# Optimization experiments

Measured on AMD Instinct MI355X. Metric: run time of the kernel, lower is better.

Reference implementation:

```python
import jax, jax.numpy as jnp
import numpy as np

NUM_LEVELS = 4
RADIUS = 4


def _avg_pool2(x):
    # x: [N, H, W] -> [N, H//2, W//2], 2x2 mean pool, stride 2 (F.avg_pool2d(corr,2,2))
    N, H, W = x.shape
    return x.reshape(N, H // 2, 2, W // 2, 2).mean(axis=(2, 4))


def _bilinear_sample(img, x, y):
    # img: [N, H, W]; x, y: [N, P] pixel coords.
    # Matches F.grid_sample(..., mode='bilinear', align_corners=True, padding_mode='zeros')
    # after the pixel->normalized->pixel round trip in bilinear_sampler (identity).
    N, H, W = img.shape
    x0 = jnp.floor(x)
    y0 = jnp.floor(y)
    wx = x - x0
    wy = y - y0
    x0i = x0.astype(jnp.int32)
    y0i = y0.astype(jnp.int32)
    flat = img.reshape(N, H * W)

    def gather(yi, xi):
        valid = (xi >= 0) & (xi <= W - 1) & (yi >= 0) & (yi <= H - 1)
        idx = jnp.clip(yi, 0, H - 1) * W + jnp.clip(xi, 0, W - 1)
        v = jnp.take_along_axis(flat, idx, axis=1)
        return jnp.where(valid, v, jnp.zeros((), img.dtype))

    v00 = gather(y0i, x0i)
    v01 = gather(y0i, x0i + 1)
    v10 = gather(y0i + 1, x0i)
    v11 = gather(y0i + 1, x0i + 1)
    return (v00 * (1 - wy) * (1 - wx) + v01 * (1 - wy) * wx
            + v10 * wy * (1 - wx) + v11 * wy * wx)


def _corr_block(fmap1, fmap2, coords):
    B, D, H, W = fmap1.shape
    # all-pairs correlation: [B, H*W, H*W] / sqrt(D)
    f1 = fmap1.reshape(B, D, H * W)
    f2 = fmap2.reshape(B, D, H * W)
    corr = jnp.einsum('bdn,bdm->bnm', f1, f2) / jnp.sqrt(jnp.asarray(D, fmap1.dtype))
    corr = corr.reshape(B * H * W, H, W)
    pyramid = [corr]
    for _ in range(NUM_LEVELS - 1):
        corr = _avg_pool2(corr)
        pyramid.append(corr)

    # coords: [B, 2, H, W] (x, y) -> [B*H*W, 2]
    c = coords.transpose(0, 2, 3, 1).reshape(B * H * W, 2)
    r = RADIUS
    d = jnp.linspace(-r, r, 2 * r + 1)
    dyg, dxg = jnp.meshgrid(d, d, indexing='ij')
    # faithful to torch: delta = stack(meshgrid(dy, dx), -1); channel 0 added to x, 1 to y
    delta = jnp.stack([dyg, dxg], axis=-1).reshape(-1, 2)  # [81, 2]

    outs = []
    for i, lvl in enumerate(pyramid):
        cl = c[:, None, :] / (2.0 ** i) + delta[None, :, :]  # [N, 81, 2]
        s = _bilinear_sample(lvl, cl[..., 0], cl[..., 1])    # [N, 81]
        outs.append(s.reshape(B, H, W, (2 * r + 1) ** 2))
    out = jnp.concatenate(outs, axis=-1)                     # [B, H, W, 4*81]
    return out.transpose(0, 3, 1, 2).astype(jnp.float32)


def setup_inputs() -> dict:
    key = jax.random.key(0)
    k1, k2, k3 = jax.random.split(key, 3)
    B, D, H, W = 2, 256, 80, 80
    fmap1 = jax.random.normal(k1, (B, D, H, W), dtype=jnp.float32)
    fmap2 = jax.random.normal(k2, (B, D, H, W), dtype=jnp.float32)
    # pixel coords in [0, W-1] x [0, H-1] (channel 0 = x, channel 1 = y)
    u = jax.random.uniform(k3, (B, 2, H, W), dtype=jnp.float32)
    scale = jnp.asarray([W - 1, H - 1], jnp.float32).reshape(1, 2, 1, 1)
    coords = u * scale
    return {"fmap1": fmap1, "fmap2": fmap2, "coords": coords}


def reference(fmap1, fmap2, coords):
    return _corr_block(fmap1, fmap2, coords)
```

## Files before the change

### kernel.cpp

```cpp
#include <hip/hip_runtime.h>


typedef _Float16 h2 __attribute__((ext_vector_type(2)));
typedef _Float16 half8 __attribute__((ext_vector_type(8)));
typedef float f32x4 __attribute__((ext_vector_type(4)));

#define HWDIM 80
#define DCH 256
#define NPIX 12800
#define NBUCKET 800
#define CHP 352

__global__ __launch_bounds__(256) void zero_k(float4* __restrict__ dst) {
    int i = blockIdx.x * 256 + threadIdx.x;
    dst[i] = make_float4(0.f, 0.f, 0.f, 0.f);
}

__global__ __launch_bounds__(256) void transpose_all(const float* __restrict__ f1,
                                                     const float* __restrict__ f2,
                                                     _Float16* __restrict__ f1h,
                                                     _Float16* __restrict__ f2p0) {
    __shared__ float tile[256][33];
    int bid = blockIdx.x;
    bool isf1 = bid < 400;
    int lb = isf1 ? bid : bid - 400;
    const float* src = isf1 ? f1 : f2;
    int b = lb / 200;
    int s0 = (lb % 200) * 32;
    int t = threadIdx.x;
    const float* sb = src + (size_t)b * DCH * (HWDIM * HWDIM);
#pragma unroll 4
    for (int k = 0; k < 32; ++k) {
        int j = t + 256 * k;
        int c = j >> 5, s = j & 31;
        tile[c][s] = sb[(size_t)c * (HWDIM * HWDIM) + s0 + s];
    }
    __syncthreads();
    int p = t & 127;
    int srow = t >> 7;
    if (isf1) {
        _Float16* db = f1h + ((size_t)b * 6400 + s0) * DCH;
#pragma unroll 4
        for (int k = 0; k < 16; ++k) {
            int s = 2 * k + srow;
            h2 v;
            v[0] = (_Float16)tile[2 * p][s];
            v[1] = (_Float16)tile[2 * p + 1][s];
            *(h2*)(db + (size_t)s * DCH + 2 * p) = v;
        }
    } else {
#pragma unroll 4
        for (int k = 0; k < 16; ++k) {
            int s = 2 * k + srow;
            int spatial = s0 + s;
            int yy = spatial / 80;
            int xx = spatial - yy * 80;
            h2 v;
            v[0] = (_Float16)tile[2 * p][s];
            v[1] = (_Float16)tile[2 * p + 1][s];
            size_t off = (size_t)b * 2073600 + (size_t)(p >> 4) * 259200
                       + ((size_t)(yy + 5) * 90 + (xx + 5)) * 32 + ((2 * p) & 31);
            *(h2*)(f2p0 + off) = v;
        }
    }
}

__global__ __launch_bounds__(256) void pools(const _Float16* __restrict__ l0,
                                             _Float16* __restrict__ l1,
                                             _Float16* __restrict__ l2,
                                             _Float16* __restrict__ l3) {
    int i = blockIdx.x * 256 + threadIdx.x;
    if (i < 409600) {
        int c2 = i & 15;
        int r = i >> 4;
        int x = r % 40; r /= 40;
        int y = r % 40; r /= 40;
        int pl = r & 7;
        int b = r >> 3;
        const h2* s = (const h2*)l0 + (size_t)b * 1036800 + (size_t)pl * 129600
                    + ((size_t)(2 * y + 5) * 90 + (2 * x + 5)) * 16 + c2;
        h2 v00 = s[0], v01 = s[16], v10 = s[90 * 16], v11 = s[90 * 16 + 16];
        float r0 = ((float)v00[0] + (float)v01[0] + (float)v10[0] + (float)v11[0]) * 0.25f;
        float r1 = ((float)v00[1] + (float)v01[1] + (float)v10[1] + (float)v11[1]) * 0.25f;
        h2 o; o[0] = (_Float16)r0; o[1] = (_Float16)r1;
        *((h2*)l1 + (size_t)b * 320000 + (size_t)pl * 40000
          + ((size_t)(y + 5) * 50 + (x + 5)) * 16 + c2) = o;
    } else if (i < 512000) {
        int j = i - 409600;
        int c2 = j & 15;
        int r = j >> 4;
        int x = r % 20; r /= 20;
        int y = r % 20; r /= 20;
        int pl = r & 7;
        int b = r >> 3;
        const h2* s = (const h2*)l0 + (size_t)b * 1036800 + (size_t)pl * 129600 + c2;
        float r0 = 0.f, r1 = 0.f;
#pragma unroll
        for (int dy = 0; dy < 4; ++dy)
#pragma unroll
            for (int dx = 0; dx < 4; ++dx) {
                h2 v = s[((size_t)(4 * y + dy + 5) * 90 + (4 * x + dx + 5)) * 16];
                r0 += (float)v[0];
                r1 += (float)v[1];
            }
        h2 o; o[0] = (_Float16)(r0 * 0.0625f); o[1] = (_Float16)(r1 * 0.0625f);
        *((h2*)l2 + (size_t)b * 115200 + (size_t)pl * 14400
          + ((size_t)(y + 5) * 30 + (x + 5)) * 16 + c2) = o;
    } else {
        int j = i - 512000;
        int c2 = j & 15;
        int r = j >> 4;
        int x = r % 10; r /= 10;
        int y = r % 10; r /= 10;
        int pl = r & 7;
        int b = r >> 3;
        const h2* s = (const h2*)l0 + (size_t)b * 1036800 + (size_t)pl * 129600 + c2;
        float r0 = 0.f, r1 = 0.f;
#pragma unroll
        for (int dy = 0; dy < 8; ++dy)
#pragma unroll
            for (int dx = 0; dx < 8; ++dx) {
                h2 v = s[((size_t)(8 * y + dy + 5) * 90 + (8 * x + dx + 5)) * 16];
                r0 += (float)v[0];
                r1 += (float)v[1];
            }
        h2 o; o[0] = (_Float16)(r0 * 0.015625f); o[1] = (_Float16)(r1 * 0.015625f);
        *((h2*)l3 + (size_t)b * 51200 + (size_t)pl * 6400
          + ((size_t)(y + 5) * 20 + (x + 5)) * 16 + c2) = o;
    }
}

static __device__ __forceinline__ int bucket_of(const float* coords, int n) {
    int b = n / 6400;
    int r = n - b * 6400;
    float cx = coords[(size_t)b * 12800 + r];
    float cy = coords[(size_t)b * 12800 + 6400 + r];
    int ix = min(max((int)floorf(cx), 0), 79);
    int iy = min(max((int)floorf(cy), 0), 79);
    return b * 400 + (iy >> 2) * 20 + (ix >> 2);
}

__global__ __launch_bounds__(1024) void bucket_k(const float* __restrict__ coords,
                                                 int* __restrict__ sortedIdxP,
                                                 int* __restrict__ rank) {
    __shared__ unsigned int histS[NBUCKET], startS[NBUCKET], curS[NBUCKET];
    __shared__ unsigned int waveSum[16];
    __shared__ unsigned int totalS;
    int t = threadIdx.x;
    if (t < NBUCKET) histS[t] = 0u;
    __syncthreads();
    int bkt[13];
#pragma unroll
    for (int i = 0; i < 13; ++i) {
        int n = i * 1024 + t;
        if (n < NPIX) {
            bkt[i] = bucket_of(coords, n);
            atomicAdd(&histS[bkt[i]], 1u);
        }
    }
    __syncthreads();
    unsigned int v = (t < NBUCKET) ? ((histS[t] + 15u) & ~15u) : 0u;
    unsigned int x = v;
#pragma unroll
    for (int d = 1; d < 64; d <<= 1) {
        unsigned int y = __shfl_up(x, d);
        if ((t & 63) >= d) x += y;
    }
    if ((t & 63) == 63) waveSum[t >> 6] = x;
    __syncthreads();
    if (t < 16) {
        unsigned int w = waveSum[t];
#pragma unroll
        for (int d = 1; d < 16; d <<= 1) {
            unsigned int y = __shfl_up(w, d);
            if (t >= d) w += y;
        }
        waveSum[t] = w;
    }
    __syncthreads();
    unsigned int incl = x + ((t >> 6) ? waveSum[(t >> 6) - 1] : 0u);
    if (t < NBUCKET) {
        unsigned int e = incl - v;
        startS[t] = e;
        curS[t] = e;
        if (t == NBUCKET - 1) totalS = incl;
    }
    __syncthreads();
#pragma unroll
    for (int i = 0; i < 13; ++i) {
        int n = i * 1024 + t;
        if (n < NPIX) {
            unsigned int pos = atomicAdd(&curS[bkt[i]], 1u);
            sortedIdxP[pos] = n;
            rank[n] = (int)pos;
        }
    }
    __syncthreads();
    if (t < NBUCKET) {
        unsigned int h = histS[t];
        if (h) {
            unsigned int pc = (h + 15u) & ~15u;
            unsigned int base = startS[t];
            int dup = sortedIdxP[base];
            for (unsigned int s = h; s < pc; ++s) sortedIdxP[base + s] = dup;
        }
    }
    for (unsigned int s = totalS + t; s < 25600u; s += 1024u) sortedIdxP[s] = -1;
}

template <int TB, int TE>
static __device__ __forceinline__ void run_tiles(
    int lane, int b,
    const _Float16* __restrict__ f2p0, const _Float16* __restrict__ f2p1,
    const _Float16* __restrict__ f2p2, const _Float16* __restrict__ f2p3,
    const int* X0cS, const int* Y0cS, const half8* bf, _Float16* G) {
#pragma unroll
    for (int tt = TB; tt < TE; ++tt) {
        const int L  = tt < 11 ? 0 : tt < 19 ? 1 : tt < 26 ? 2 : 3;
        const int rt = tt - (L == 0 ? 0 : L == 1 ? 11 : L == 2 ? 19 : 26);
        const int Ww = L == 0 ? 13 : L == 1 ? 11 : 10;
        const int MT = L == 0 ? 169 : L == 1 ? 121 : 100;
        const int MAG = L == 0 ? 161320 : L == 1 ? 190652 : 209716;
        const int Wp = L == 0 ? 90 : L == 1 ? 50 : L == 2 ? 30 : 20;
        const int PS = L == 0 ? 259200 : L == 1 ? 80000 : L == 2 ? 28800 : 12800;
        const int PB = L == 0 ? 2073600 : L == 1 ? 640000 : L == 2 ? 230400 : 102400;
        const int GO = L == 0 ? 0 : L == 1 ? 176 : L == 2 ? 304 : 416;
        const _Float16* f2L = (L == 0 ? f2p0 : L == 1 ? f2p1 : L == 2 ? f2p2 : f2p3);
        const _Float16* f2b = f2L + (size_t)b * PB
                            + ((size_t)(Y0cS[L] + 5) * Wp + (X0cS[L] + 5)) * 32;
        int m = min(rt * 16 + (lane & 15), MT - 1);
        int my = (m * MAG) >> 21;
        int mx = m - my * Ww;
        const float4* ap = (const float4*)(f2b + (size_t)(my * Wp + mx) * 32)
                         + (lane >> 4);
        half8 av[8];
#pragma unroll
        for (int kk = 0; kk < 8; ++kk)
            av[kk] = __builtin_bit_cast(half8, ap[kk * (PS / 8)]);
        __builtin_amdgcn_sched_barrier(0);
        f32x4 acc0 = {0.f, 0.f, 0.f, 0.f};
        f32x4 acc1 = {0.f, 0.f, 0.f, 0.f};
#pragma unroll
        for (int kk = 0; kk < 8; kk += 2) {
            acc0 = __builtin_amdgcn_mfma_f32_16x16x32_f16(av[kk], bf[kk], acc0, 0, 0, 0);
            acc1 = __builtin_amdgcn_mfma_f32_16x16x32_f16(av[kk + 1], bf[kk + 1], acc1, 0, 0, 0);
        }
        int gr = GO + rt * 16 + (lane >> 4) * 4;
#pragma unroll
        for (int r = 0; r < 4; ++r)
            G[(gr + r) * 17 + (lane & 15)] = (_Float16)(acc0[r] + acc1[r]);
    }
}

__global__ __launch_bounds__(512, 4) void corr_mfma(
    const _Float16* __restrict__ f1h,
    const _Float16* __restrict__ f2p0, const _Float16* __restrict__ f2p1,
    const _Float16* __restrict__ f2p2, const _Float16* __restrict__ f2p3,
    const float* __restrict__ coords, const int* __restrict__ sortedIdxP,
    _Float16* __restrict__ scratch) {
    __shared__ _Float16 G[528 * 17];
    __shared__ _Float16 f1S[16 * 264];
    __shared__ float fxS[4][16], fyS[4][16];
    __shared__ int lxS[4][16], lyS[4][16];
    __shared__ int X0cS[4], Y0cS[4], bS;

    int pphys = blockIdx.x;
    int l = (pphys & 7) * 200 + (pphys >> 3);
    int tid = threadIdx.x;
    if (sortedIdxP[l * 16] < 0) return;
    int lane = tid & 63;
    int wave = tid >> 6;

    {
        int px = tid >> 5, q = tid & 31;
        int n = sortedIdxP[l * 16 + px];
        const float4* src = (const float4*)(f1h + (size_t)n * DCH);
        *((float4*)(f1S + px * 264) + q) = src[q];
    }
    if (tid < 64) {
        int px = tid & 15, Lt = tid >> 4;
        int n = sortedIdxP[l * 16 + px];
        int b = n / 6400;
        int r = n - b * 6400;
        float cx = coords[(size_t)b * 12800 + r];
        float cy = coords[(size_t)b * 12800 + 6400 + r];
        float ls = 1.0f / (float)(1 << Lt);
        float cxl = cx * ls, cyl = cy * ls;
        float fxf = floorf(cxl), fyf = floorf(cyl);
        int X0 = (int)fxf - 4, Y0 = (int)fyf - 4;
        int ix = min(max((int)floorf(cx), 0), 79);
        int iy = min(max((int)floorf(cy), 0), 79);
        int X0c = (((ix >> 2) * 4) >> Lt) - 4;
        int Y0c = (((iy >> 2) * 4) >> Lt) - 4;
        lxS[Lt][px] = min(max(X0 - X0c, 0), 3);
        lyS[Lt][px] = min(max(Y0 - Y0c, 0), 3);
        fxS[Lt][px] = cxl - fxf;
        fyS[Lt][px] = cyl - fyf;
        X0cS[Lt] = X0c;
        Y0cS[Lt] = Y0c;
        if (tid == 0) bS = sortedIdxP[l * 16] / 6400;
    }
    __syncthreads();
    int b = bS;

    half8 bf[8];
#pragma unroll
    for (int kk = 0; kk < 8; ++kk)
        bf[kk] = *(const half8*)(f1S + (lane & 15) * 264 + ((lane >> 4) + 4 * kk) * 8);

    if      (wave == 0) run_tiles<0, 5>(lane, b, f2p0, f2p1, f2p2, f2p3, X0cS, Y0cS, bf, G);
    else if (wave == 1) run_tiles<5, 9>(lane, b, f2p0, f2p1, f2p2, f2p3, X0cS, Y0cS, bf, G);
    else if (wave == 2) run_tiles<9, 13>(lane, b, f2p0, f2p1, f2p2, f2p3, X0cS, Y0cS, bf, G);
    else if (wave == 3) run_tiles<13, 17>(lane, b, f2p0, f2p1, f2p2, f2p3, X0cS, Y0cS, bf, G);
    else if (wave == 4) run_tiles<17, 21>(lane, b, f2p0, f2p1, f2p2, f2p3, X0cS, Y0cS, bf, G);
    else if (wave == 5) run_tiles<21, 25>(lane, b, f2p0, f2p1, f2p2, f2p3, X0cS, Y0cS, bf, G);
    else if (wave == 6) run_tiles<25, 29>(lane, b, f2p0, f2p1, f2p2, f2p3, X0cS, Y0cS, bf, G);
    else                run_tiles<29, 33>(lane, b, f2p0, f2p1, f2p2, f2p3, X0cS, Y0cS, bf, G);
    __syncthreads();

    _Float16* sc = scratch + (size_t)l * 16 * CHP;
    for (int idx = tid; idx < 5184; idx += 512) {
        int k2 = idx >> 4, x = idx & 15;
        int Le = (k2 * 810) >> 16;
        int k = k2 - Le * 81;
        int Ww = Le == 0 ? 13 : Le == 1 ? 11 : 10;
        int GO = Le == 0 ? 0 : Le == 1 ? 176 : Le == 2 ? 304 : 416;
        int a = (k * 57) >> 9;
        int c = k - 9 * a;
        int gx = lxS[Le][x] + a, gy = lyS[Le][x] + c;
        int m00 = GO + gy * Ww + gx;
        float fx = fxS[Le][x], fy = fyS[Le][x];
        float t00 = (float)G[m00 * 17 + x];
        float t01 = (float)G[(m00 + 1) * 17 + x];
        float t10 = (float)G[(m00 + Ww) * 17 + x];
        float t11 = (float)G[(m00 + Ww + 1) * 17 + x];
        float v = ((1.f - fy) * ((1.f - fx) * t00 + fx * t01)
                 + fy * ((1.f - fx) * t10 + fx * t11)) * 0.0625f;
        sc[x * CHP + k2] = (_Float16)v;
    }
}

__global__ __launch_bounds__(256) void unsort_t(const _Float16* __restrict__ scratch,
                                                const int* __restrict__ rank,
                                                float* __restrict__ out) {
    __shared__ _Float16 lds[64][40];
    int blk = blockIdx.x;
    int b = blk / 100;
    int nl0 = (blk % 100) * 64;
    int t = threadIdx.x;
    int p = t >> 2, j = t & 3;
    int n = blk * 64 + p;
    int rk = rank[n];
    const float4* src = (const float4*)(scratch + (size_t)rk * CHP);
    int px = t & 63, iq = t >> 6;

    for (int c = 0; c < 11; ++c) {
        float4 f4 = src[c * 4 + j];
        *(float4*)(&lds[p][j * 8]) = f4;
        __syncthreads();
#pragma unroll
        for (int w = 0; w < 8; ++w) {
            int i = w * 4 + iq;
            int ch = c * 32 + i;
            if (ch < 324)
                out[((size_t)b * 324 + ch) * 6400 + nl0 + px] = (float)lds[px][i];
        }
        __syncthreads();
    }
}

extern "C" void kernel_launch(void* const* d_in, const int* in_sizes, int n_in,
                              void* d_out, int out_size, void* d_ws, size_t ws_size,
                              hipStream_t stream) {
    const float* fmap1 = (const float*)d_in[0];
    const float* fmap2 = (const float*)d_in[1];
    const float* coords = (const float*)d_in[2];
    float* out = (float*)d_out;
    char* ws = (char*)d_ws;

    _Float16* f1h  = (_Float16*)(ws);
    _Float16* f2p0 = (_Float16*)(ws + 6553600);
    _Float16* f2p1 = (_Float16*)(ws + 14848000);
    _Float16* f2p2 = (_Float16*)(ws + 17408000);
    _Float16* f2p3 = (_Float16*)(ws + 18329600);
    int* sortedIdxP = (int*)(ws + 18739200);
    int* rank       = (int*)(ws + 18841600);
    _Float16* scratch = (_Float16*)(ws + 18892800);

    zero_k<<<dim3(2975), dim3(256), 0, stream>>>((float4*)f2p0);

    transpose_all<<<dim3(800), dim3(256), 0, stream>>>(fmap1, fmap2, f1h, f2p0);
    pools<<<dim3(2100), dim3(256), 0, stream>>>(f2p0, f2p1, f2p2, f2p3);
    bucket_k<<<dim3(1), dim3(1024), 0, stream>>>(coords, sortedIdxP, rank);
    corr_mfma<<<dim3(1600), dim3(512), 0, stream>>>(f1h, f2p0, f2p1, f2p2, f2p3,
                                                    coords, sortedIdxP, scratch);
    unsort_t<<<dim3(200), dim3(256), 0, stream>>>(scratch, rank, out);
}
```

Measured before the change: 98.22 us.

## Stage f2 planes through LDS with double-buffered async loads per pyramid level

Replaces per-wave direct global loads of all eight K-planes with cooperative global_load_lds staging into a swizzled double-buffered LDS plane, processing pyramid levels one at a time. The G buffer shrinks to a single level and launch bounds ask for more blocks per CU, trading register-held operands for LDS traffic and many more block-wide barriers. The sampling epilogue is split per level. The aim is better overlap of global loads with MFMA and higher occupancy, at the cost of extra synchronization and idle waves on levels with fewer tiles.

```diff
diff --git a/kernel.cpp b/kernel.cpp
--- a/kernel.cpp
+++ b/kernel.cpp
@@ -208,57 +208,113 @@
     for (unsigned int s = totalS + t; s < 25600u; s += 1024u) sortedIdxP[s] = -1;
 }
 
-template <int TB, int TE>
-static __device__ __forceinline__ void run_tiles(
-    int lane, int b,
-    const _Float16* __restrict__ f2p0, const _Float16* __restrict__ f2p1,
-    const _Float16* __restrict__ f2p2, const _Float16* __restrict__ f2p3,
-    const int* X0cS, const int* Y0cS, const half8* bf, _Float16* G) {
-#pragma unroll
-    for (int tt = TB; tt < TE; ++tt) {
-        const int L  = tt < 11 ? 0 : tt < 19 ? 1 : tt < 26 ? 2 : 3;
-        const int rt = tt - (L == 0 ? 0 : L == 1 ? 11 : L == 2 ? 19 : 26);
-        const int Ww = L == 0 ? 13 : L == 1 ? 11 : 10;
-        const int MT = L == 0 ? 169 : L == 1 ? 121 : 100;
-        const int MAG = L == 0 ? 161320 : L == 1 ? 190652 : 209716;
-        const int Wp = L == 0 ? 90 : L == 1 ? 50 : L == 2 ? 30 : 20;
-        const int PS = L == 0 ? 259200 : L == 1 ? 80000 : L == 2 ? 28800 : 12800;
-        const int PB = L == 0 ? 2073600 : L == 1 ? 640000 : L == 2 ? 230400 : 102400;
-        const int GO = L == 0 ? 0 : L == 1 ? 176 : L == 2 ? 304 : 416;
-        const _Float16* f2L = (L == 0 ? f2p0 : L == 1 ? f2p1 : L == 2 ? f2p2 : f2p3);
-        const _Float16* f2b = f2L + (size_t)b * PB
-                            + ((size_t)(Y0cS[L] + 5) * Wp + (X0cS[L] + 5)) * 32;
-        int m = min(rt * 16 + (lane & 15), MT - 1);
-        int my = (m * MAG) >> 21;
-        int mx = m - my * Ww;
-        const float4* ap = (const float4*)(f2b + (size_t)(my * Wp + mx) * 32)
-                         + (lane >> 4);
-        half8 av[8];
-#pragma unroll
-        for (int kk = 0; kk < 8; ++kk)
-            av[kk] = __builtin_bit_cast(half8, ap[kk * (PS / 8)]);
-        __builtin_amdgcn_sched_barrier(0);
-        f32x4 acc0 = {0.f, 0.f, 0.f, 0.f};
-        f32x4 acc1 = {0.f, 0.f, 0.f, 0.f};
-#pragma unroll
-        for (int kk = 0; kk < 8; kk += 2) {
-            acc0 = __builtin_amdgcn_mfma_f32_16x16x32_f16(av[kk], bf[kk], acc0, 0, 0, 0);
-            acc1 = __builtin_amdgcn_mfma_f32_16x16x32_f16(av[kk + 1], bf[kk + 1], acc1, 0, 0, 0);
-        }
-        int gr = GO + rt * 16 + (lane >> 4) * 4;
-#pragma unroll
-        for (int r = 0; r < 4; ++r)
-            G[(gr + r) * 17 + (lane & 15)] = (_Float16)(acc0[r] + acc1[r]);
-    }
-}
-
-__global__ __launch_bounds__(512, 4) void corr_mfma(
+template <int L>
+static __device__ __forceinline__ void stage_plane(int tid, int wave, int kk,
+                                                   const _Float16* __restrict__ f2b,
+                                                   char* buf) {
+    const int Ww = L == 0 ? 13 : L == 1 ? 11 : 10;
+    const int MT = L == 0 ? 169 : L == 1 ? 121 : 100;
+    const int MAG = L == 0 ? 161320 : L == 1 ? 190652 : 209716;
+    const int Wp = L == 0 ? 90 : L == 1 ? 50 : L == 2 ? 30 : 20;
+    const int PSB = 2 * (L == 0 ? 259200 : L == 1 ? 80000 : L == 2 ? 28800 : 12800);
+    const int NS = MT * 4;
+#pragma unroll
+    for (int p = 0; p < (NS + 511) / 512; ++p) {
+        int s = p * 512 + tid;
+        if (s < NS) {
+            int r = s >> 2, c = s & 3;
+            int my = (r * MAG) >> 21;
+            int mx = r - my * Ww;
+            int cc = c ^ (r & 3);
+            const char* g = (const char*)f2b + (my * Wp + mx) * 64 + cc * 16 + kk * PSB;
+            char* l = buf + (p * 512 + wave * 64) * 16;
+            __builtin_amdgcn_global_load_lds(
+                (const __attribute__((address_space(1))) void*)g,
+                (__attribute__((address_space(3))) void*)l, 16, 0, 0);
+        }
+    }
+}
+
+template <int L>
+static __device__ __forceinline__ void run_level(
+    int tid, int lane, int wave, int b,
+    const _Float16* __restrict__ f2pL,
+    const int* X0cS, const int* Y0cS,
+    const float (*fxS)[16], const float (*fyS)[16],
+    const int (*lxS)[16], const int (*lyS)[16],
+    const _Float16* f1S, char (*planeB)[176 * 64], _Float16* G,
+    _Float16* __restrict__ sc) {
+    const int Ww = L == 0 ? 13 : L == 1 ? 11 : 10;
+    const int NT = L == 0 ? 11 : L == 1 ? 8 : 7;
+    const int MT = L == 0 ? 169 : L == 1 ? 121 : 100;
+    const int Wp = L == 0 ? 90 : L == 1 ? 50 : L == 2 ? 30 : 20;
+    const int PB = L == 0 ? 2073600 : L == 1 ? 640000 : L == 2 ? 230400 : 102400;
+    const _Float16* f2b = f2pL + (size_t)b * PB
+                        + ((size_t)(Y0cS[L] + 5) * Wp + (X0cS[L] + 5)) * 32;
+    bool has0 = wave < NT;
+    bool has1 = (wave + 8) < NT;
+    int ch = lane >> 4;
+    int r0 = min(wave * 16 + (lane & 15), MT - 1);
+    int r1 = min((wave + 8) * 16 + (lane & 15), MT - 1);
+    int la0 = (r0 * 4 + (ch ^ (r0 & 3))) * 16;
+    int la1 = (r1 * 4 + (ch ^ (r1 & 3))) * 16;
+
+    f32x4 acc0 = {0.f, 0.f, 0.f, 0.f};
+    f32x4 acc1 = {0.f, 0.f, 0.f, 0.f};
+    stage_plane<L>(tid, wave, 0, f2b, planeB[0]);
+    __syncthreads();
+#pragma unroll
+    for (int kk = 0; kk < 8; ++kk) {
+        if (kk < 7) stage_plane<L>(tid, wave, kk + 1, f2b, planeB[(kk + 1) & 1]);
+        half8 bfk = *(const half8*)(f1S + (lane & 15) * 264 + (ch + 4 * kk) * 8);
+        const char* pb = planeB[kk & 1];
+        if (has0) {
+            half8 a0 = *(const half8*)(pb + la0);
+            acc0 = __builtin_amdgcn_mfma_f32_16x16x32_f16(a0, bfk, acc0, 0, 0, 0);
+        }
+        if (has1) {
+            half8 a1 = *(const half8*)(pb + la1);
+            acc1 = __builtin_amdgcn_mfma_f32_16x16x32_f16(a1, bfk, acc1, 0, 0, 0);
+        }
+        __syncthreads();
+    }
+    if (has0) {
+        int gr = wave * 16 + ch * 4;
+#pragma unroll
+        for (int r = 0; r < 4; ++r) G[(gr + r) * 17 + (lane & 15)] = (_Float16)acc0[r];
+    }
+    if (has1) {
+        int gr = (wave + 8) * 16 + ch * 4;
+#pragma unroll
+        for (int r = 0; r < 4; ++r) G[(gr + r) * 17 + (lane & 15)] = (_Float16)acc1[r];
+    }
+    __syncthreads();
+    for (int idx = tid; idx < 16 * 81; idx += 512) {
+        int x = (idx * 12946) >> 20;
+        int k = idx - x * 81;
+        int a = (k * 57) >> 9;
+        int c = k - 9 * a;
+        int gx = lxS[L][x] + a, gy = lyS[L][x] + c;
+        int m00 = gy * Ww + gx;
+        float fx = fxS[L][x], fy = fyS[L][x];
+        float t00 = (float)G[m00 * 17 + x];
+        float t01 = (float)G[(m00 + 1) * 17 + x];
+        float t10 = (float)G[(m00 + Ww) * 17 + x];
+        float t11 = (float)G[(m00 + Ww + 1) * 17 + x];
+        float v = ((1.f - fy) * ((1.f - fx) * t00 + fx * t01)
+                 + fy * ((1.f - fx) * t10 + fx * t11)) * 0.0625f;
+        sc[x * CHP + L * 81 + k] = (_Float16)v;
+    }
+}
+
+__global__ __launch_bounds__(512, 8) void corr_mfma(
     const _Float16* __restrict__ f1h,
     const _Float16* __restrict__ f2p0, const _Float16* __restrict__ f2p1,
     const _Float16* __restrict__ f2p2, const _Float16* __restrict__ f2p3,
     const float* __restrict__ coords, const int* __restrict__ sortedIdxP,
     _Float16* __restrict__ scratch) {
-    __shared__ _Float16 G[528 * 17];
+    __shared__ __align__(16) char planeB[2][176 * 64];
+    __shared__ _Float16 G[176 * 17];
     __shared__ _Float16 f1S[16 * 264];
     __shared__ float fxS[4][16], fyS[4][16];
     __shared__ int lxS[4][16], lyS[4][16];
@@ -302,42 +358,12 @@
     }
     __syncthreads();
     int b = bS;
-
-    half8 bf[8];
-#pragma unroll
-    for (int kk = 0; kk < 8; ++kk)
-        bf[kk] = *(const half8*)(f1S + (lane & 15) * 264 + ((lane >> 4) + 4 * kk) * 8);
-
-    if      (wave == 0) run_tiles<0, 5>(lane, b, f2p0, f2p1, f2p2, f2p3, X0cS, Y0cS, bf, G);
-    else if (wave == 1) run_tiles<5, 9>(lane, b, f2p0, f2p1, f2p2, f2p3, X0cS, Y0cS, bf, G);
-    else if (wave == 2) run_tiles<9, 13>(lane, b, f2p0, f2p1, f2p2, f2p3, X0cS, Y0cS, bf, G);
-    else if (wave == 3) run_tiles<13, 17>(lane, b, f2p0, f2p1, f2p2, f2p3, X0cS, Y0cS, bf, G);
-    else if (wave == 4) run_tiles<17, 21>(lane, b, f2p0, f2p1, f2p2, f2p3, X0cS, Y0cS, bf, G);
-    else if (wave == 5) run_tiles<21, 25>(lane, b, f2p0, f2p1, f2p2, f2p3, X0cS, Y0cS, bf, G);
-    else if (wave == 6) run_tiles<25, 29>(lane, b, f2p0, f2p1, f2p2, f2p3, X0cS, Y0cS, bf, G);
-    else                run_tiles<29, 33>(lane, b, f2p0, f2p1, f2p2, f2p3, X0cS, Y0cS, bf, G);
-    __syncthreads();
-
     _Float16* sc = scratch + (size_t)l * 16 * CHP;
-    for (int idx = tid; idx < 5184; idx += 512) {
-        int k2 = idx >> 4, x = idx & 15;
-        int Le = (k2 * 810) >> 16;
-        int k = k2 - Le * 81;
-        int Ww = Le == 0 ? 13 : Le == 1 ? 11 : 10;
-        int GO = Le == 0 ? 0 : Le == 1 ? 176 : Le == 2 ? 304 : 416;
-        int a = (k * 57) >> 9;
-        int c = k - 9 * a;
-        int gx = lxS[Le][x] + a, gy = lyS[Le][x] + c;
-        int m00 = GO + gy * Ww + gx;
-        float fx = fxS[Le][x], fy = fyS[Le][x];
-        float t00 = (float)G[m00 * 17 + x];
-        float t01 = (float)G[(m00 + 1) * 17 + x];
-        float t10 = (float)G[(m00 + Ww) * 17 + x];
-        float t11 = (float)G[(m00 + Ww + 1) * 17 + x];
-        float v = ((1.f - fy) * ((1.f - fx) * t00 + fx * t01)
-                 + fy * ((1.f - fx) * t10 + fx * t11)) * 0.0625f;
-        sc[x * CHP + k2] = (_Float16)v;
-    }
+
+    run_level<0>(tid, lane, wave, b, f2p0, X0cS, Y0cS, fxS, fyS, lxS, lyS, f1S, planeB, G, sc);
+    run_level<1>(tid, lane, wave, b, f2p1, X0cS, Y0cS, fxS, fyS, lxS, lyS, f1S, planeB, G, sc);
+    run_level<2>(tid, lane, wave, b, f2p2, X0cS, Y0cS, fxS, fyS, lxS, lyS, f1S, planeB, G, sc);
+    run_level<3>(tid, lane, wave, b, f2p3, X0cS, Y0cS, fxS, fyS, lxS, lyS, f1S, planeB, G, sc);
 }
 
 __global__ __launch_bounds__(256) void unsort_t(const _Float16* __restrict__ scratch,
```

Measured after the change: 90.86 us, median of 2. 7.5% less time.
